# Kernel optimization log

Hardware: AMD Instinct MI355X
Metric: run time of the kernel (lower is better)

## Reference

```python
import jax, jax.numpy as jnp
import numpy as np

B = 4096      # number of boards
H = 256       # n_hidden
SCALE = 0.0625  # 1/sqrt(H)
N_POLICY = 1858


def setup_inputs() -> dict:
    key = jax.random.key(0)
    ks = jax.random.split(key, 10)
    w_s = 1.0 / 16.0  # keep activations well-scaled
    return {
        "x": jax.random.normal(ks[0], (B * 64, H), jnp.float32),
        "w1": jax.random.normal(ks[1], (H, H), jnp.float32) * w_s,
        "b1": jax.random.normal(ks[2], (H,), jnp.float32) * w_s,
        "w2": jax.random.normal(ks[3], (H, H), jnp.float32) * w_s,
        "b2": jax.random.normal(ks[4], (H,), jnp.float32) * w_s,
        "w3": jax.random.normal(ks[5], (H, H), jnp.float32) * w_s,
        "b3": jax.random.normal(ks[6], (H,), jnp.float32) * w_s,
        "w4": jax.random.normal(ks[7], (4, H), jnp.float32) * w_s,
        "gather_idx": jax.random.randint(ks[8], (N_POLICY,), 0, 4288, jnp.int32),
    }


def reference(x, w1, b1, w2, b2, w3, b3, w4, gather_idx):
    out = jax.nn.relu(x @ w1.T + b1)                      # (B*64, H)
    q = (out @ w2.T + b2).reshape(-1, 64, H)              # (B, 64, H)
    k = (out @ w3.T + b3).reshape(-1, 64, H)              # (B, 64, H)
    logits = jnp.einsum("bqh,bkh->bqk", q, k) * SCALE     # (B, 64, 64)

    # promotion offsets from 8th-rank keys
    promo_keys = k[:, 56:64, :]                           # (B, 8, H)
    offs = jnp.einsum("bsh,ph->bps", promo_keys, w4)      # (B, 4, 8)
    offs = offs[:, :3, :] + offs[:, 3:4, :]               # (B, 3, 8) q/r/b + knight base
    off24 = jnp.transpose(offs, (0, 2, 1)).reshape(-1, 1, 24)  # (B,1,24) piece-fastest

    # knight promotion move logits: rank7 -> rank8 block
    n_promo = logits[:, 48:56, 56:64].reshape(-1, 64, 1)  # (B, 64, 1)
    n_promo = jnp.broadcast_to(n_promo, (n_promo.shape[0], 64, 3)).reshape(-1, 8, 24)

    promo = (off24 + n_promo).reshape(-1, 3, 64)          # (B, 3, 64)

    full = jnp.concatenate([logits, promo], axis=1).reshape(-1, 4288)  # (B, 4288)
    return jnp.take(full, gather_idx, axis=1)             # (B, 1858)
```

## Files before the change

kernel.cpp:

```cpp
#include <hip/hip_runtime.h>


typedef __bf16 bf16_t;
typedef __bf16 bf16x8 __attribute__((ext_vector_type(8)));
typedef float  f32x4  __attribute__((ext_vector_type(4)));

#define PSCALE 0.0625f
#define NPOL   1858
#define MFMA(a,b,c) __builtin_amdgcn_mfma_f32_16x16x32_bf16(a, b, c, 0, 0, 0)


__global__ void prep_w1(const float* __restrict__ w1, bf16_t* __restrict__ wfA) {
    int i = blockIdx.x * 256 + threadIdx.x;
    int j = i & 7, lane = (i >> 3) & 63, t = (i >> 9) & 7, n = (i >> 12) & 15;
    int row = n * 16 + (lane & 15);
    int col = t * 32 + (lane >> 4) * 8 + j;
    wfA[i] = (bf16_t)w1[row * 256 + col];
}

__global__ void prep_mat(const float* __restrict__ w2,
                         const float* __restrict__ w3,
                         bf16_t* __restrict__ wfM) {
    int m1 = blockIdx.x, m2 = threadIdx.x;
    float acc = 0.f;
    #pragma unroll 8
    for (int h = 0; h < 256; ++h)
        acc += w2[h * 256 + m1] * w3[h * 256 + m2];
    int t = m1 >> 5, quad = (m1 >> 3) & 3, j = m1 & 7;
    int n = m2 >> 4, l15 = m2 & 15;
    wfM[(((n * 8 + t) * 64) + (quad * 16 + l15)) * 8 + j] = (bf16_t)acc;
}

__global__ void prep_vecs(const float* __restrict__ w2,
                          const float* __restrict__ w3,
                          const float* __restrict__ b2,
                          const float* __restrict__ b3,
                          const float* __restrict__ w4,
                          float* __restrict__ flt) {
    int m = threadIdx.x;
    float c2 = 0.f, vv = 0.f, p0 = 0.f, p1 = 0.f, p2 = 0.f, p3 = 0.f;
    for (int h = 0; h < 256; ++h) {
        float w3h = w3[h * 256 + m];
        c2 += b2[h] * w3h;
        p0 += w4[h] * w3h;
        p1 += w4[256 + h] * w3h;
        p2 += w4[512 + h] * w3h;
        p3 += w4[768 + h] * w3h;
        vv += w2[h * 256 + m] * b3[h];
    }
    flt[m]        = c2;
    flt[256 + m]  = vv;
    flt[512 + m]  = p0;
    flt[768 + m]  = p1;
    flt[1024 + m] = p2;
    flt[1280 + m] = p3;
    if (m < 4) {
        float pb = 0.f;
        for (int h = 0; h < 256; ++h) pb += w4[m * 256 + h] * b3[h];
        flt[1536 + m] = pb;
    }
    if (m == 0) {
        float s = 0.f;
        for (int h = 0; h < 256; ++h) s += b2[h] * b3[h];
        flt[1540] = s;
    }
}


template <bool USE_WS>
__device__ __forceinline__ bf16x8 wfrag(const bf16_t* __restrict__ wl,
                                        const float* __restrict__ w,
                                        int n, int t, int lane) {
    if constexpr (USE_WS) {
        return *(const bf16x8*)(wl + (((n * 8 + t) * 64 + lane) << 3));
    } else {
        int l15 = lane & 15, quad = lane >> 4;
        const float* p = w + (n * 16 + l15) * 256 + t * 32 + quad * 8;
        f32x4 lo = *(const f32x4*)p;
        f32x4 hi = *(const f32x4*)(p + 4);
        bf16x8 v;
        v[0] = (bf16_t)lo[0]; v[1] = (bf16_t)lo[1];
        v[2] = (bf16_t)lo[2]; v[3] = (bf16_t)lo[3];
        v[4] = (bf16_t)hi[0]; v[5] = (bf16_t)hi[1];
        v[6] = (bf16_t)hi[2]; v[7] = (bf16_t)hi[3];
        return v;
    }
}

__device__ __forceinline__ int ks_off(int row, int col) {
    return ((row << 9) + (col << 1)) ^ ((row & 7) << 4);
}

__device__ __forceinline__ bf16x8 cvt8(const float* __restrict__ p) {
    f32x4 lo = *(const f32x4*)p;
    f32x4 hi = *(const f32x4*)(p + 4);
    bf16x8 v;
    v[0] = (bf16_t)lo[0]; v[1] = (bf16_t)lo[1];
    v[2] = (bf16_t)lo[2]; v[3] = (bf16_t)lo[3];
    v[4] = (bf16_t)hi[0]; v[5] = (bf16_t)hi[1];
    v[6] = (bf16_t)hi[2]; v[7] = (bf16_t)hi[3];
    return v;
}

__device__ __forceinline__ void mfma16(const bf16x8* inA, const bf16x8* inB,
                                       const bf16x8* w, f32x4& s0, f32x4& s1) {
    f32x4 a00 = {0.f,0.f,0.f,0.f}, a01 = {0.f,0.f,0.f,0.f};
    f32x4 a10 = {0.f,0.f,0.f,0.f}, a11 = {0.f,0.f,0.f,0.f};
    #pragma unroll
    for (int t = 0; t < 8; t += 2) {
        a00 = MFMA(inA[t],     w[t],     a00);
        a10 = MFMA(inB[t],     w[t],     a10);
        a01 = MFMA(inA[t + 1], w[t + 1], a01);
        a11 = MFMA(inB[t + 1], w[t + 1], a11);
    }
    s0 = a00 + a01;
    s1 = a10 + a11;
}

template <bool RELU>
__device__ __forceinline__ void tile_store2(unsigned char* __restrict__ u_lds,
                                            const f32x4& sA, const f32x4& sB,
                                            float bv, int n,
                                            int quad, int l15, int R) {
    #pragma unroll
    for (int r2 = 0; r2 < 4; ++r2) {
        int off = ks_off(R + quad * 4 + r2, n * 16 + l15);
        float vA = sA[r2] + bv, vB = sB[r2] + bv;
        if (RELU) { vA = fmaxf(vA, 0.f); vB = fmaxf(vB, 0.f); }
        *(bf16_t*)(u_lds + off)         = (bf16_t)vA;
        *(bf16_t*)(u_lds + 32768 + off) = (bf16_t)vB;
    }
}

template <bool USE_WS, bool RELU>
__device__ __forceinline__ void layer2b(const bf16x8* inA, const bf16x8* inB,
                                        const bf16_t* __restrict__ wl,
                                        const float* __restrict__ wraw,
                                        const float* __restrict__ bias,
                                        unsigned char* __restrict__ u_lds,
                                        int lane, int quad, int l15, int R) {
    bf16x8 w0[8], w1[8];
    #pragma unroll
    for (int t = 0; t < 8; ++t)
        w0[t] = wfrag<USE_WS>(wl, wraw, 0, t, lane);

    #pragma unroll
    for (int np = 0; np < 8; ++np) {
        const int nE = 2 * np, nO = nE + 1;

        #pragma unroll
        for (int t = 0; t < 8; ++t)
            w1[t] = wfrag<USE_WS>(wl, wraw, nO, t, lane);
        {
            f32x4 sA, sB;
            mfma16(inA, inB, w0, sA, sB);
            tile_store2<RELU>(u_lds, sA, sB, bias[nE * 16 + l15], nE, quad, l15, R);
        }

        if (np < 7) {
            #pragma unroll
            for (int t = 0; t < 8; ++t)
                w0[t] = wfrag<USE_WS>(wl, wraw, nE + 2, t, lane);
        }
        {
            f32x4 sA, sB;
            mfma16(inA, inB, w1, sA, sB);
            tile_store2<RELU>(u_lds, sA, sB, bias[nO * 16 + l15], nO, quad, l15, R);
        }
    }
}

__global__ __launch_bounds__(256, 1)
void policy_fused(const float* __restrict__ x,
                  const bf16_t* __restrict__ wfA,
                  const bf16_t* __restrict__ wfM,
                  const float* __restrict__ flt,
                  const float* __restrict__ b1,
                  const int*   __restrict__ gidx,
                  float* __restrict__ out,
                  int nbat) {
    __shared__ __align__(16) unsigned char u_lds[2 * 32768];
    __shared__ __align__(16) bf16_t qscr[4][2][16 * 40];
    __shared__ float promoLDS[2][4][8];
    __shared__ float patchLDS[2][8][8];

    const int tid  = threadIdx.x;
    const int lane = tid & 63;
    const int wv   = tid >> 6;
    const int quad = lane >> 4;
    const int l15  = lane & 15;
    const int R    = wv * 16;

    const int bat0 = blockIdx.x * 2;
    const bool has1 = (bat0 + 1) < nbat;
    const int bat1 = has1 ? bat0 + 1 : bat0;

    bf16x8 xaA[8], xaB[8];
    {
        const float* xr0 = x + ((size_t)bat0 * 64 + R + l15) * 256;
        const float* xr1 = x + ((size_t)bat1 * 64 + R + l15) * 256;
        #pragma unroll
        for (int t = 0; t < 8; ++t) {
            xaA[t] = cvt8(xr0 + t * 32 + quad * 8);
            xaB[t] = cvt8(xr1 + t * 32 + quad * 8);
        }
    }

    layer2b<true, true>(xaA, xaB, wfA, nullptr, b1, u_lds, lane, quad, l15, R);
    bf16x8 oaA[8], oaB[8];
    #pragma unroll
    for (int t = 0; t < 8; ++t) {
        int off = ks_off(R + l15, t * 32 + quad * 8);
        oaA[t] = *(const bf16x8*)(u_lds + off);
        oaB[t] = *(const bf16x8*)(u_lds + 32768 + off);
    }

    float qbA = flt[1540], qbB = qbA;
    {
        const float* vvec = flt + 256;
        #pragma unroll
        for (int t = 0; t < 8; ++t) {
            f32x4 va = *(const f32x4*)(vvec + t * 32 + quad * 8);
            f32x4 vb = *(const f32x4*)(vvec + t * 32 + quad * 8 + 4);
            qbA += (float)oaA[t][0]*va[0] + (float)oaA[t][1]*va[1]
                 + (float)oaA[t][2]*va[2] + (float)oaA[t][3]*va[3]
                 + (float)oaA[t][4]*vb[0] + (float)oaA[t][5]*vb[1]
                 + (float)oaA[t][6]*vb[2] + (float)oaA[t][7]*vb[3];
            qbB += (float)oaB[t][0]*va[0] + (float)oaB[t][1]*va[1]
                 + (float)oaB[t][2]*va[2] + (float)oaB[t][3]*va[3]
                 + (float)oaB[t][4]*vb[0] + (float)oaB[t][5]*vb[1]
                 + (float)oaB[t][6]*vb[2] + (float)oaB[t][7]*vb[3];
        }
        qbA += __shfl_xor(qbA, 16);  qbA += __shfl_xor(qbA, 32);
        qbB += __shfl_xor(qbB, 16);  qbB += __shfl_xor(qbB, 32);
    }

    __syncthreads();

    f32x4 laA[4], laB[4];
    #pragma unroll
    for (int n = 0; n < 4; ++n) {
        laA[n] = (f32x4){0.f,0.f,0.f,0.f};
        laB[n] = (f32x4){0.f,0.f,0.f,0.f};
    }
    {
        bf16_t* qsA = &qscr[wv][0][0];
        bf16_t* qsB = &qscr[wv][1][0];
        bf16x8 wc[8], wn[8];
        #pragma unroll
        for (int t = 0; t < 8; ++t)
            wc[t] = wfrag<true>(wfM, nullptr, 0, t, lane);

        #pragma unroll
        for (int t8 = 0; t8 < 8; ++t8) {
            const int n0 = 2 * t8, n1 = n0 + 1;

            #pragma unroll
            for (int t = 0; t < 8; ++t)
                wn[t] = wfrag<true>(wfM, nullptr, n1, t, lane);
            {
                f32x4 sA, sB;
                mfma16(oaA, oaB, wc, sA, sB);
                float bv = flt[n0 * 16 + l15];
                #pragma unroll
                for (int r2 = 0; r2 < 4; ++r2) {
                    int qo = (quad * 4 + r2) * 40 + l15;
                    qsA[qo] = (bf16_t)(sA[r2] + bv);
                    qsB[qo] = (bf16_t)(sB[r2] + bv);
                }
            }

            if (t8 < 7) {
                #pragma unroll
                for (int t = 0; t < 8; ++t)
                    wc[t] = wfrag<true>(wfM, nullptr, n0 + 2, t, lane);
            }
            {
                f32x4 sA, sB;
                mfma16(oaA, oaB, wn, sA, sB);
                float bv = flt[n1 * 16 + l15];
                #pragma unroll
                for (int r2 = 0; r2 < 4; ++r2) {
                    int qo = (quad * 4 + r2) * 40 + 16 + l15;
                    qsA[qo] = (bf16_t)(sA[r2] + bv);
                    qsB[qo] = (bf16_t)(sB[r2] + bv);
                }
            }

            bf16x8 qaA = *(const bf16x8*)(qsA + l15 * 40 + quad * 8);
            bf16x8 qaB = *(const bf16x8*)(qsB + l15 * 40 + quad * 8);
            #pragma unroll
            for (int np = 0; np < 4; ++np) {
                int ko = ks_off(np * 16 + l15, t8 * 32 + quad * 8);
                bf16x8 kA = *(const bf16x8*)(u_lds + ko);
                bf16x8 kB = *(const bf16x8*)(u_lds + 32768 + ko);
                laA[np] = MFMA(qaA, kA, laA[np]);
                laB[np] = MFMA(qaB, kB, laB[np]);
            }
        }
    }

    float qbra[4], qbrb[4];
    #pragma unroll
    for (int r2 = 0; r2 < 4; ++r2) {
        qbra[r2] = __shfl(qbA, quad * 4 + r2);
        qbrb[r2] = __shfl(qbB, quad * 4 + r2);
    }

    {
        int s = lane >> 3, seg = lane & 7;
        const float* wrow = flt + 512 + wv * 256;
        #pragma unroll
        for (int b = 0; b < 2; ++b) {
            const unsigned char* kb = u_lds + b * 32768;
            float p = 0.f;
            #pragma unroll
            for (int m = 0; m < 4; ++m) {
                bf16x8 kv = *(const bf16x8*)(kb + ks_off(56 + s, seg * 32 + m * 8));
                f32x4 wa = *(const f32x4*)(wrow + seg * 32 + m * 8);
                f32x4 wb = *(const f32x4*)(wrow + seg * 32 + m * 8 + 4);
                p += (float)kv[0] * wa[0] + (float)kv[1] * wa[1]
                   + (float)kv[2] * wa[2] + (float)kv[3] * wa[3]
                   + (float)kv[4] * wb[0] + (float)kv[5] * wb[1]
                   + (float)kv[6] * wb[2] + (float)kv[7] * wb[3];
            }
            p += __shfl_down(p, 4);
            p += __shfl_down(p, 2);
            p += __shfl_down(p, 1);
            if (seg == 0) promoLDS[b][wv][s] = p + flt[1536 + wv];
        }
    }

    if (wv == 3 && quad < 2 && l15 >= 8) {
        #pragma unroll
        for (int r2 = 0; r2 < 4; ++r2) {
            patchLDS[0][quad * 4 + r2][l15 - 8] = (laA[3][r2] + qbra[r2]) * PSCALE;
            patchLDS[1][quad * 4 + r2][l15 - 8] = (laB[3][r2] + qbrb[r2]) * PSCALE;
        }
    }

    __syncthreads();

    float* fb0 = (float*)u_lds;
    float* fb1 = (float*)(u_lds + 32768);
    #pragma unroll
    for (int n = 0; n < 4; ++n) {
        #pragma unroll
        for (int r2 = 0; r2 < 4; ++r2) {
            int idx = (R + quad * 4 + r2) * 64 + n * 16 + l15;
            fb0[idx] = (laA[n][r2] + qbra[r2]) * PSCALE;
            fb1[idx] = (laB[n][r2] + qbrb[r2]) * PSCALE;
        }
    }

    if (tid < 192) {
        int u = tid >> 6, vv2 = tid & 63;
        int mm = u * 64 + vv2;
        int r_ = mm / 24, c_ = mm - r_ * 24;
        int c3 = c_ / 3, cp = c_ - c3 * 3;
        fb0[(64 + u) * 64 + vv2] =
            promoLDS[0][cp][c3] + promoLDS[0][3][c3] + patchLDS[0][r_][c3];
        fb1[(64 + u) * 64 + vv2] =
            promoLDS[1][cp][c3] + promoLDS[1][3][c3] + patchLDS[1][r_][c3];
    }

    __syncthreads();

    {
        float* orow0 = out + (size_t)bat0 * NPOL;
        float* orow1 = out + (size_t)(bat0 + 1) * NPOL;
        int   idxv[8];
        float v0[8], v1[8];
        #pragma unroll
        for (int i = 0; i < 8; ++i) {
            int g = tid + i * 256;
            idxv[i] = (g < NPOL) ? gidx[g] : 0;
        }
        #pragma unroll
        for (int i = 0; i < 8; ++i) {
            v0[i] = fb0[idxv[i]];
            v1[i] = fb1[idxv[i]];
        }
        #pragma unroll
        for (int i = 0; i < 8; ++i) {
            int g = tid + i * 256;
            if (g < NPOL) {
                orow0[g] = v0[i];
                if (has1) orow1[g] = v1[i];
            }
        }
    }
}

__global__ __launch_bounds__(256, 2)
void policy_main(const float* __restrict__ x,
                 const float* __restrict__ w1,
                 const float* __restrict__ w2,
                 const float* __restrict__ w3,
                 const float* __restrict__ b1,
                 const float* __restrict__ b2,
                 const float* __restrict__ b3,
                 const float* __restrict__ w4,
                 const int*   __restrict__ gidx,
                 float* __restrict__ out,
                 int nbat) {
    __shared__ __align__(16) unsigned char u_lds[2 * 32768];
    __shared__ __align__(16) bf16_t qscr[4][2][16 * 40];
    __shared__ float promoLDS[2][4][8];
    __shared__ float patchLDS[2][8][8];

    const int tid  = threadIdx.x;
    const int lane = tid & 63;
    const int wv   = tid >> 6;
    const int quad = lane >> 4;
    const int l15  = lane & 15;
    const int R    = wv * 16;

    const int bat0 = blockIdx.x * 2;
    const bool has1 = (bat0 + 1) < nbat;
    const int bat1 = has1 ? bat0 + 1 : bat0;

    bf16x8 xaA[8], xaB[8];
    {
        const float* xr0 = x + ((size_t)bat0 * 64 + R + l15) * 256;
        const float* xr1 = x + ((size_t)bat1 * 64 + R + l15) * 256;
        #pragma unroll
        for (int t = 0; t < 8; ++t) {
            xaA[t] = cvt8(xr0 + t * 32 + quad * 8);
            xaB[t] = cvt8(xr1 + t * 32 + quad * 8);
        }
    }

    layer2b<false, true>(xaA, xaB, nullptr, w1, b1, u_lds, lane, quad, l15, R);
    bf16x8 oaA[8], oaB[8];
    #pragma unroll
    for (int t = 0; t < 8; ++t) {
        int off = ks_off(R + l15, t * 32 + quad * 8);
        oaA[t] = *(const bf16x8*)(u_lds + off);
        oaB[t] = *(const bf16x8*)(u_lds + 32768 + off);
    }

    layer2b<false, false>(oaA, oaB, nullptr, w3, b3, u_lds, lane, quad, l15, R);

    __syncthreads();

    f32x4 laA[4], laB[4];
    #pragma unroll
    for (int n = 0; n < 4; ++n) {
        laA[n] = (f32x4){0.f,0.f,0.f,0.f};
        laB[n] = (f32x4){0.f,0.f,0.f,0.f};
    }
    {
        bf16_t* qsA = &qscr[wv][0][0];
        bf16_t* qsB = &qscr[wv][1][0];
        bf16x8 wc[8], wn[8];
        #pragma unroll
        for (int t = 0; t < 8; ++t)
            wc[t] = wfrag<false>(nullptr, w2, 0, t, lane);

        #pragma unroll
        for (int t8 = 0; t8 < 8; ++t8) {
            const int n0 = 2 * t8, n1 = n0 + 1;
            #pragma unroll
            for (int t = 0; t < 8; ++t)
                wn[t] = wfrag<false>(nullptr, w2, n1, t, lane);
            {
                f32x4 sA, sB;
                mfma16(oaA, oaB, wc, sA, sB);
                float bv = b2[n0 * 16 + l15];
                #pragma unroll
                for (int r2 = 0; r2 < 4; ++r2) {
                    int qo = (quad * 4 + r2) * 40 + l15;
                    qsA[qo] = (bf16_t)(sA[r2] + bv);
                    qsB[qo] = (bf16_t)(sB[r2] + bv);
                }
            }
            if (t8 < 7) {
                #pragma unroll
                for (int t = 0; t < 8; ++t)
                    wc[t] = wfrag<false>(nullptr, w2, n0 + 2, t, lane);
            }
            {
                f32x4 sA, sB;
                mfma16(oaA, oaB, wn, sA, sB);
                float bv = b2[n1 * 16 + l15];
                #pragma unroll
                for (int r2 = 0; r2 < 4; ++r2) {
                    int qo = (quad * 4 + r2) * 40 + 16 + l15;
                    qsA[qo] = (bf16_t)(sA[r2] + bv);
                    qsB[qo] = (bf16_t)(sB[r2] + bv);
                }
            }
            bf16x8 qaA = *(const bf16x8*)(qsA + l15 * 40 + quad * 8);
            bf16x8 qaB = *(const bf16x8*)(qsB + l15 * 40 + quad * 8);
            #pragma unroll
            for (int np = 0; np < 4; ++np) {
                int ko = ks_off(np * 16 + l15, t8 * 32 + quad * 8);
                bf16x8 kA = *(const bf16x8*)(u_lds + ko);
                bf16x8 kB = *(const bf16x8*)(u_lds + 32768 + ko);
                laA[np] = MFMA(qaA, kA, laA[np]);
                laB[np] = MFMA(qaB, kB, laB[np]);
            }
        }
    }

    {
        int s = lane >> 3, seg = lane & 7;
        const float* wrow = w4 + wv * 256;
        #pragma unroll
        for (int b = 0; b < 2; ++b) {
            const unsigned char* kb = u_lds + b * 32768;
            float p = 0.f;
            #pragma unroll
            for (int m = 0; m < 4; ++m) {
                bf16x8 kv = *(const bf16x8*)(kb + ks_off(56 + s, seg * 32 + m * 8));
                f32x4 wa = *(const f32x4*)(wrow + seg * 32 + m * 8);
                f32x4 wb = *(const f32x4*)(wrow + seg * 32 + m * 8 + 4);
                p += (float)kv[0] * wa[0] + (float)kv[1] * wa[1]
                   + (float)kv[2] * wa[2] + (float)kv[3] * wa[3]
                   + (float)kv[4] * wb[0] + (float)kv[5] * wb[1]
                   + (float)kv[6] * wb[2] + (float)kv[7] * wb[3];
            }
            p += __shfl_down(p, 4);
            p += __shfl_down(p, 2);
            p += __shfl_down(p, 1);
            if (seg == 0) promoLDS[b][wv][s] = p;
        }
    }

    if (wv == 3 && quad < 2 && l15 >= 8) {
        #pragma unroll
        for (int r2 = 0; r2 < 4; ++r2) {
            patchLDS[0][quad * 4 + r2][l15 - 8] = laA[3][r2] * PSCALE;
            patchLDS[1][quad * 4 + r2][l15 - 8] = laB[3][r2] * PSCALE;
        }
    }

    __syncthreads();

    float* fb0 = (float*)u_lds;
    float* fb1 = (float*)(u_lds + 32768);
    #pragma unroll
    for (int n = 0; n < 4; ++n) {
        #pragma unroll
        for (int r2 = 0; r2 < 4; ++r2) {
            int idx = (R + quad * 4 + r2) * 64 + n * 16 + l15;
            fb0[idx] = laA[n][r2] * PSCALE;
            fb1[idx] = laB[n][r2] * PSCALE;
        }
    }

    if (tid < 192) {
        int u = tid >> 6, vv2 = tid & 63;
        int mm = u * 64 + vv2;
        int r_ = mm / 24, c_ = mm - r_ * 24;
        int c3 = c_ / 3, cp = c_ - c3 * 3;
        fb0[(64 + u) * 64 + vv2] =
            promoLDS[0][cp][c3] + promoLDS[0][3][c3] + patchLDS[0][r_][c3];
        fb1[(64 + u) * 64 + vv2] =
            promoLDS[1][cp][c3] + promoLDS[1][3][c3] + patchLDS[1][r_][c3];
    }

    __syncthreads();

    {
        float* orow0 = out + (size_t)bat0 * NPOL;
        float* orow1 = out + (size_t)(bat0 + 1) * NPOL;
        int   idxv[8];
        float v0[8], v1[8];
        #pragma unroll
        for (int i = 0; i < 8; ++i) {
            int g = tid + i * 256;
            idxv[i] = (g < NPOL) ? gidx[g] : 0;
        }
        #pragma unroll
        for (int i = 0; i < 8; ++i) {
            v0[i] = fb0[idxv[i]];
            v1[i] = fb1[idxv[i]];
        }
        #pragma unroll
        for (int i = 0; i < 8; ++i) {
            int g = tid + i * 256;
            if (g < NPOL) {
                orow0[g] = v0[i];
                if (has1) orow1[g] = v1[i];
            }
        }
    }
}

extern "C" void kernel_launch(void* const* d_in, const int* in_sizes, int n_in,
                              void* d_out, int out_size, void* d_ws, size_t ws_size,
                              hipStream_t stream) {
    const float* x    = (const float*)d_in[0];
    const float* w1   = (const float*)d_in[1];
    const float* b1   = (const float*)d_in[2];
    const float* w2   = (const float*)d_in[3];
    const float* b2   = (const float*)d_in[4];
    const float* w3   = (const float*)d_in[5];
    const float* b3   = (const float*)d_in[6];
    const float* w4   = (const float*)d_in[7];
    const int*   gidx = (const int*)d_in[8];
    float* out = (float*)d_out;

    int nbat = in_sizes[0] / (64 * 256);
    int nblk = (nbat + 1) / 2;
    const size_t ws_needed = 262144 + 8192;

    if (ws_size >= ws_needed) {
        bf16_t* wfA = (bf16_t*)d_ws;
        bf16_t* wfM = wfA + 65536;
        float*  flt = (float*)((char*)d_ws + 262144);
        prep_w1  <<<256, 256, 0, stream>>>(w1, wfA);
        prep_mat <<<256, 256, 0, stream>>>(w2, w3, wfM);
        prep_vecs<<<1,   256, 0, stream>>>(w2, w3, b2, b3, w4, flt);
        policy_fused<<<nblk, 256, 0, stream>>>(
            x, wfA, wfM, flt, b1, gidx, out, nbat);
    } else {
        policy_main<<<nblk, 256, 0, stream>>>(
            x, w1, w2, w3, b1, b2, b3, w4, gidx, out, nbat);
    }
}
```

Before: 539.8 us.

## Cut register pressure to allow two blocks per CU

Raises launch bounds from one to two blocks per CU. To fit that, the weight double-buffering is split into half-tile (4-fragment) prefetches, and the layer-1 output activations are re-read from LDS inside the q-projection instead of being held in registers. The qb scalar is staged through a small LDS array rather than kept live across the loop. The aim is more resident waves to hide memory and MFMA latency, at the cost of extra LDS reads and shorter prefetch distance, with a risk of spills.

```diff
diff --git a/kernel.cpp b/kernel.cpp
--- a/kernel.cpp
+++ b/kernel.cpp
@@ -117,6 +117,28 @@
     s1 = a10 + a11;
 }
 
+__device__ __forceinline__ void qtile_lds(const unsigned char* __restrict__ u_lds,
+                                          const bf16x8* w, f32x4& s0, f32x4& s1,
+                                          int quad, int l15, int R) {
+    f32x4 a00 = {0.f,0.f,0.f,0.f}, a01 = {0.f,0.f,0.f,0.f};
+    f32x4 a10 = {0.f,0.f,0.f,0.f}, a11 = {0.f,0.f,0.f,0.f};
+    #pragma unroll
+    for (int t = 0; t < 8; t += 2) {
+        int oE = ks_off(R + l15, t * 32 + quad * 8);
+        int oO = ks_off(R + l15, (t + 1) * 32 + quad * 8);
+        bf16x8 xA0 = *(const bf16x8*)(u_lds + oE);
+        bf16x8 xB0 = *(const bf16x8*)(u_lds + 32768 + oE);
+        bf16x8 xA1 = *(const bf16x8*)(u_lds + oO);
+        bf16x8 xB1 = *(const bf16x8*)(u_lds + 32768 + oO);
+        a00 = MFMA(xA0, w[t],     a00);
+        a10 = MFMA(xB0, w[t],     a10);
+        a01 = MFMA(xA1, w[t + 1], a01);
+        a11 = MFMA(xB1, w[t + 1], a11);
+    }
+    s0 = a00 + a01;
+    s1 = a10 + a11;
+}
+
 template <bool RELU>
 __device__ __forceinline__ void tile_store2(unsigned char* __restrict__ u_lds,
                                             const f32x4& sA, const f32x4& sB,
@@ -139,38 +161,41 @@
                                         const float* __restrict__ bias,
                                         unsigned char* __restrict__ u_lds,
                                         int lane, int quad, int l15, int R) {
-    bf16x8 w0[8], w1[8];
-    #pragma unroll
-    for (int t = 0; t < 8; ++t)
-        w0[t] = wfrag<USE_WS>(wl, wraw, 0, t, lane);
-
-    #pragma unroll
-    for (int np = 0; np < 8; ++np) {
-        const int nE = 2 * np, nO = nE + 1;
-
-        #pragma unroll
-        for (int t = 0; t < 8; ++t)
-            w1[t] = wfrag<USE_WS>(wl, wraw, nO, t, lane);
-        {
-            f32x4 sA, sB;
-            mfma16(inA, inB, w0, sA, sB);
-            tile_store2<RELU>(u_lds, sA, sB, bias[nE * 16 + l15], nE, quad, l15, R);
-        }
-
-        if (np < 7) {
-            #pragma unroll
-            for (int t = 0; t < 8; ++t)
-                w0[t] = wfrag<USE_WS>(wl, wraw, nE + 2, t, lane);
-        }
-        {
-            f32x4 sA, sB;
-            mfma16(inA, inB, w1, sA, sB);
-            tile_store2<RELU>(u_lds, sA, sB, bias[nO * 16 + l15], nO, quad, l15, R);
-        }
-    }
-}
-
-__global__ __launch_bounds__(256, 1)
+    bf16x8 wA[4], wB[4];
+    #pragma unroll
+    for (int t = 0; t < 4; ++t)
+        wA[t] = wfrag<USE_WS>(wl, wraw, 0, t, lane);
+
+    #pragma unroll
+    for (int n = 0; n < 16; ++n) {
+        #pragma unroll
+        for (int t = 0; t < 4; ++t)
+            wB[t] = wfrag<USE_WS>(wl, wraw, n, 4 + t, lane);
+
+        f32x4 aA0 = {0.f,0.f,0.f,0.f}, aA1 = {0.f,0.f,0.f,0.f};
+        f32x4 aB0 = {0.f,0.f,0.f,0.f}, aB1 = {0.f,0.f,0.f,0.f};
+        aA0 = MFMA(inA[0], wA[0], aA0);  aB0 = MFMA(inB[0], wA[0], aB0);
+        aA1 = MFMA(inA[1], wA[1], aA1);  aB1 = MFMA(inB[1], wA[1], aB1);
+        aA0 = MFMA(inA[2], wA[2], aA0);  aB0 = MFMA(inB[2], wA[2], aB0);
+        aA1 = MFMA(inA[3], wA[3], aA1);  aB1 = MFMA(inB[3], wA[3], aB1);
+
+        if (n < 15) {
+            #pragma unroll
+            for (int t = 0; t < 4; ++t)
+                wA[t] = wfrag<USE_WS>(wl, wraw, n + 1, t, lane);
+        }
+
+        aA0 = MFMA(inA[4], wB[0], aA0);  aB0 = MFMA(inB[4], wB[0], aB0);
+        aA1 = MFMA(inA[5], wB[1], aA1);  aB1 = MFMA(inB[5], wB[1], aB1);
+        aA0 = MFMA(inA[6], wB[2], aA0);  aB0 = MFMA(inB[6], wB[2], aB0);
+        aA1 = MFMA(inA[7], wB[3], aA1);  aB1 = MFMA(inB[7], wB[3], aB1);
+
+        tile_store2<RELU>(u_lds, aA0 + aA1, aB0 + aB1,
+                          bias[n * 16 + l15], n, quad, l15, R);
+    }
+}
+
+__global__ __launch_bounds__(256, 2)
 void policy_fused(const float* __restrict__ x,
                   const bf16_t* __restrict__ wfA,
                   const bf16_t* __restrict__ wfM,
@@ -183,6 +208,7 @@
     __shared__ __align__(16) bf16_t qscr[4][2][16 * 40];
     __shared__ float promoLDS[2][4][8];
     __shared__ float patchLDS[2][8][8];
+    __shared__ float qbLDS[2][64];
 
     const int tid  = threadIdx.x;
     const int lane = tid & 63;
@@ -207,33 +233,38 @@
     }
 
     layer2b<true, true>(xaA, xaB, wfA, nullptr, b1, u_lds, lane, quad, l15, R);
-    bf16x8 oaA[8], oaB[8];
-    #pragma unroll
-    for (int t = 0; t < 8; ++t) {
-        int off = ks_off(R + l15, t * 32 + quad * 8);
-        oaA[t] = *(const bf16x8*)(u_lds + off);
-        oaB[t] = *(const bf16x8*)(u_lds + 32768 + off);
-    }
-
-    float qbA = flt[1540], qbB = qbA;
-    {
+
+    {
+        float qbA = flt[1540], qbB = qbA;
         const float* vvec = flt + 256;
         #pragma unroll
         for (int t = 0; t < 8; ++t) {
+            int off = ks_off(R + l15, t * 32 + quad * 8);
+            bf16x8 oA = *(const bf16x8*)(u_lds + off);
+            bf16x8 oB = *(const bf16x8*)(u_lds + 32768 + off);
             f32x4 va = *(const f32x4*)(vvec + t * 32 + quad * 8);
             f32x4 vb = *(const f32x4*)(vvec + t * 32 + quad * 8 + 4);
-            qbA += (float)oaA[t][0]*va[0] + (float)oaA[t][1]*va[1]
-                 + (float)oaA[t][2]*va[2] + (float)oaA[t][3]*va[3]
-                 + (float)oaA[t][4]*vb[0] + (float)oaA[t][5]*vb[1]
-                 + (float)oaA[t][6]*vb[2] + (float)oaA[t][7]*vb[3];
-            qbB += (float)oaB[t][0]*va[0] + (float)oaB[t][1]*va[1]
-                 + (float)oaB[t][2]*va[2] + (float)oaB[t][3]*va[3]
-                 + (float)oaB[t][4]*vb[0] + (float)oaB[t][5]*vb[1]
-                 + (float)oaB[t][6]*vb[2] + (float)oaB[t][7]*vb[3];
+            qbA += (float)oA[0]*va[0] + (float)oA[1]*va[1]
+                 + (float)oA[2]*va[2] + (float)oA[3]*va[3]
+                 + (float)oA[4]*vb[0] + (float)oA[5]*vb[1]
+                 + (float)oA[6]*vb[2] + (float)oA[7]*vb[3];
+            qbB += (float)oB[0]*va[0] + (float)oB[1]*va[1]
+                 + (float)oB[2]*va[2] + (float)oB[3]*va[3]
+                 + (float)oB[4]*vb[0] + (float)oB[5]*vb[1]
+                 + (float)oB[6]*vb[2] + (float)oB[7]*vb[3];
         }
         qbA += __shfl_xor(qbA, 16);  qbA += __shfl_xor(qbA, 32);
         qbB += __shfl_xor(qbB, 16);  qbB += __shfl_xor(qbB, 32);
-    }
+        if (lane < 16) {
+            qbLDS[0][R + lane] = qbA;
+            qbLDS[1][R + lane] = qbB;
+        }
+    }
+
+    bf16x8 wc[8], wn[8];
+    #pragma unroll
+    for (int t = 0; t < 8; ++t)
+        wc[t] = wfrag<true>(wfM, nullptr, 0, t, lane);
 
     __syncthreads();
 
@@ -246,10 +277,6 @@
     {
         bf16_t* qsA = &qscr[wv][0][0];
         bf16_t* qsB = &qscr[wv][1][0];
-        bf16x8 wc[8], wn[8];
-        #pragma unroll
-        for (int t = 0; t < 8; ++t)
-            wc[t] = wfrag<true>(wfM, nullptr, 0, t, lane);
 
         #pragma unroll
         for (int t8 = 0; t8 < 8; ++t8) {
@@ -260,7 +287,7 @@
                 wn[t] = wfrag<true>(wfM, nullptr, n1, t, lane);
             {
                 f32x4 sA, sB;
-                mfma16(oaA, oaB, wc, sA, sB);
+                qtile_lds(u_lds, wc, sA, sB, quad, l15, R);
                 float bv = flt[n0 * 16 + l15];
                 #pragma unroll
                 for (int r2 = 0; r2 < 4; ++r2) {
@@ -277,7 +304,7 @@
             }
             {
                 f32x4 sA, sB;
-                mfma16(oaA, oaB, wn, sA, sB);
+                qtile_lds(u_lds, wn, sA, sB, quad, l15, R);
                 float bv = flt[n1 * 16 + l15];
                 #pragma unroll
                 for (int r2 = 0; r2 < 4; ++r2) {
@@ -303,8 +330,8 @@
     float qbra[4], qbrb[4];
     #pragma unroll
     for (int r2 = 0; r2 < 4; ++r2) {
-        qbra[r2] = __shfl(qbA, quad * 4 + r2);
-        qbrb[r2] = __shfl(qbB, quad * 4 + r2);
+        qbra[r2] = qbLDS[0][R + quad * 4 + r2];
+        qbrb[r2] = qbLDS[1][R + quad * 4 + r2];
     }
 
     {
@@ -453,20 +480,32 @@
     {
         bf16_t* qsA = &qscr[wv][0][0];
         bf16_t* qsB = &qscr[wv][1][0];
-        bf16x8 wc[8], wn[8];
-        #pragma unroll
-        for (int t = 0; t < 8; ++t)
-            wc[t] = wfrag<false>(nullptr, w2, 0, t, lane);
+        bf16x8 wA[4], wB[4];
+        #pragma unroll
+        for (int t = 0; t < 4; ++t)
+            wA[t] = wfrag<false>(nullptr, w2, 0, t, lane);
 
         #pragma unroll
         for (int t8 = 0; t8 < 8; ++t8) {
             const int n0 = 2 * t8, n1 = n0 + 1;
             #pragma unroll
-            for (int t = 0; t < 8; ++t)
-                wn[t] = wfrag<false>(nullptr, w2, n1, t, lane);
+            for (int t = 0; t < 4; ++t)
+                wB[t] = wfrag<false>(nullptr, w2, n0, 4 + t, lane);
             {
-                f32x4 sA, sB;
-                mfma16(oaA, oaB, wc, sA, sB);
+                f32x4 cA0 = {0.f,0.f,0.f,0.f}, cA1 = {0.f,0.f,0.f,0.f};
+                f32x4 cB0 = {0.f,0.f,0.f,0.f}, cB1 = {0.f,0.f,0.f,0.f};
+                cA0 = MFMA(oaA[0], wA[0], cA0);  cB0 = MFMA(oaB[0], wA[0], cB0);
+                cA1 = MFMA(oaA[1], wA[1], cA1);  cB1 = MFMA(oaB[1], wA[1], cB1);
+                cA0 = MFMA(oaA[2], wA[2], cA0);  cB0 = MFMA(oaB[2], wA[2], cB0);
+                cA1 = MFMA(oaA[3], wA[3], cA1);  cB1 = MFMA(oaB[3], wA[3], cB1);
+                #pragma unroll
+                for (int t = 0; t < 4; ++t)
+                    wA[t] = wfrag<false>(nullptr, w2, n1, t, lane);
+                cA0 = MFMA(oaA[4], wB[0], cA0);  cB0 = MFMA(oaB[4], wB[0], cB0);
+                cA1 = MFMA(oaA[5], wB[1], cA1);  cB1 = MFMA(oaB[5], wB[1], cB1);
+                cA0 = MFMA(oaA[6], wB[2], cA0);  cB0 = MFMA(oaB[6], wB[2], cB0);
+                cA1 = MFMA(oaA[7], wB[3], cA1);  cB1 = MFMA(oaB[7], wB[3], cB1);
+                f32x4 sA = cA0 + cA1, sB = cB0 + cB1;
                 float bv = b2[n0 * 16 + l15];
                 #pragma unroll
                 for (int r2 = 0; r2 < 4; ++r2) {
@@ -475,14 +514,26 @@
                     qsB[qo] = (bf16_t)(sB[r2] + bv);
                 }
             }
-            if (t8 < 7) {
-                #pragma unroll
-                for (int t = 0; t < 8; ++t)
-                    wc[t] = wfrag<false>(nullptr, w2, n0 + 2, t, lane);
-            }
+            #pragma unroll
+            for (int t = 0; t < 4; ++t)
+                wB[t] = wfrag<false>(nullptr, w2, n1, 4 + t, lane);
             {
-                f32x4 sA, sB;
-                mfma16(oaA, oaB, wn, sA, sB);
+                f32x4 cA0 = {0.f,0.f,0.f,0.f}, cA1 = {0.f,0.f,0.f,0.f};
+                f32x4 cB0 = {0.f,0.f,0.f,0.f}, cB1 = {0.f,0.f,0.f,0.f};
+                cA0 = MFMA(oaA[0], wA[0], cA0);  cB0 = MFMA(oaB[0], wA[0], cB0);
+                cA1 = MFMA(oaA[1], wA[1], cA1);  cB1 = MFMA(oaB[1], wA[1], cB1);
+                cA0 = MFMA(oaA[2], wA[2], cA0);  cB0 = MFMA(oaB[2], wA[2], cB0);
+                cA1 = MFMA(oaA[3], wA[3], cA1);  cB1 = MFMA(oaB[3], wA[3], cB1);
+                if (t8 < 7) {
+                    #pragma unroll
+                    for (int t = 0; t < 4; ++t)
+                        wA[t] = wfrag<false>(nullptr, w2, n0 + 2, t, lane);
+                }
+                cA0 = MFMA(oaA[4], wB[0], cA0);  cB0 = MFMA(oaB[4], wB[0], cB0);
+                cA1 = MFMA(oaA[5], wB[1], cA1);  cB1 = MFMA(oaB[5], wB[1], cB1);
+                cA0 = MFMA(oaA[6], wB[2], cA0);  cB0 = MFMA(oaB[6], wB[2], cB0);
+                cA1 = MFMA(oaA[7], wB[3], cA1);  cB1 = MFMA(oaB[7], wB[3], cB1);
+                f32x4 sA = cA0 + cA1, sB = cB0 + cB1;
                 float bv = b2[n1 * 16 + l15];
                 #pragma unroll
                 for (int r2 = 0; r2 < 4; ++r2) {
```

Measured after the change: 523.9 us. -3.0%, faster.
